# Optimization experiments

Measured on AMD Instinct MI355X. Metric: run time of the kernel, lower is better.

## Reference

```python
import jax, jax.numpy as jnp
import numpy as np

NUM_HEADS = 12
TEMPORAL_RES = 8


def _ln(x, g, b, eps=1e-5):
    mu = jnp.mean(x, axis=-1, keepdims=True)
    var = jnp.mean((x - mu) ** 2, axis=-1, keepdims=True)
    return (x - mu) * jax.lax.rsqrt(var + eps) * g + b


def setup_inputs() -> dict:
    key = jax.random.key(0)
    ks = jax.random.split(key, 8)
    s = 0.02
    d = 768
    inp = {
        'box_tensors': jax.random.uniform(ks[0], (16, 16, 10, 4), dtype=jnp.float32),
        'box_categories': jax.random.normal(ks[1], (16, 10, d), dtype=jnp.float32) * s,
        'w1': jax.random.normal(ks[2], (4, d // 2), dtype=jnp.float32) * s,
        'w2': jax.random.normal(ks[3], (d // 2, d), dtype=jnp.float32) * s,
        'ln1_g': jnp.ones((d,), jnp.float32),
        'ln1_b': jnp.zeros((d,), jnp.float32),
        'wqkv': jax.random.normal(ks[4], (d, 3 * d), dtype=jnp.float32) * s,
        'wo': jax.random.normal(ks[5], (d, d), dtype=jnp.float32) * s,
        'bo': jnp.zeros((d,), jnp.float32),
        'ln2_g': jnp.ones((d,), jnp.float32),
        'ln2_b': jnp.zeros((d,), jnp.float32),
        'wfc1': jax.random.normal(ks[6], (d, 4 * d), dtype=jnp.float32) * s,
        'bfc1': jnp.zeros((4 * d,), jnp.float32),
        'wfc2': jax.random.normal(ks[7], (4 * d, d), dtype=jnp.float32) * s,
        'bfc2': jnp.zeros((d,), jnp.float32),
        'H': 14,
        'W': 14,
    }
    return inp


def _forward(box_tensors, box_categories, w1, w2, ln1_g, ln1_b, wqkv, wo, bo,
             ln2_g, ln2_b, wfc1, bfc1, wfc2, bfc2, H, W):
    B, T, O, _ = box_tensors.shape
    d = box_categories.shape[-1]
    # coord -> feature MLP (no biases), then pos-emb add
    h = jax.nn.relu(box_tensors @ w1)
    x = jax.nn.relu(h @ w2)                      # [B,T,O,d]
    x = x + box_categories[None]                 # broadcast over batch
    L = T * O
    x = x.reshape(B, L, d)
    # --- self-attention block (pre-LN ViT style) ---
    hn = _ln(x, ln1_g, ln1_b)
    qkv = (hn @ wqkv).reshape(B, L, 3, NUM_HEADS, d // NUM_HEADS)
    q, k, v = qkv[:, :, 0], qkv[:, :, 1], qkv[:, :, 2]   # [B,L,h,dh]
    scale = 1.0 / jnp.sqrt(jnp.asarray(d // NUM_HEADS, x.dtype))
    att = jnp.einsum('bqhd,bkhd->bhqk', q, k) * scale
    att = jax.nn.softmax(att, axis=-1)
    o = jnp.einsum('bhqk,bkhd->bqhd', att, v).reshape(B, L, d)
    x = x + (o @ wo + bo)
    hn = _ln(x, ln2_g, ln2_b)
    x = x + (jax.nn.gelu(hn @ wfc1 + bfc1, approximate=False) @ wfc2 + bfc2)
    feats = x.reshape(B, T, O, d)
    # --- box2spatial layout scatter: sum each object's feature into grid cells inside its box ---
    x1 = jnp.minimum(box_tensors[..., 0], box_tensors[..., 2])
    x2 = jnp.maximum(box_tensors[..., 0], box_tensors[..., 2])
    y1 = jnp.minimum(box_tensors[..., 1], box_tensors[..., 3])
    y2 = jnp.maximum(box_tensors[..., 1], box_tensors[..., 3])
    cy = (jnp.arange(H, dtype=x.dtype) + 0.5) / H    # [H]
    cx = (jnp.arange(W, dtype=x.dtype) + 0.5) / W    # [W]
    in_y = (cy[None, None, None, :] >= y1[..., None]) & (cy[None, None, None, :] <= y2[..., None])  # [B,T,O,H]
    in_x = (cx[None, None, None, :] >= x1[..., None]) & (cx[None, None, None, :] <= x2[..., None])  # [B,T,O,W]
    mask = (in_y[..., :, None] & in_x[..., None, :]).astype(x.dtype)  # [B,T,O,H,W]
    grid = jnp.einsum('btohw,btod->bthwd', mask, feats)               # [B,T,H,W,d]
    # temporal avg pooling to TEMPORAL_RES frames
    Tr = T // TEMPORAL_RES
    if Tr > 1:
        grid = grid.reshape(B, T // Tr, Tr, H, W, d).mean(axis=2)
    return grid.reshape(B, -1, d)                 # [B, T'*H*W, d]


def reference(box_tensors, box_categories, w1, w2, ln1_g, ln1_b, wqkv, wo, bo,
              ln2_g, ln2_b, wfc1, bfc1, wfc2, bfc2, H, W):
    return _forward(box_tensors, box_categories, w1, w2, ln1_g, ln1_b, wqkv, wo, bo,
                    ln2_g, ln2_b, wfc1, bfc1, wfc2, bfc2, H, W)
```

## Files before the change

kernel.cpp:

```cpp
#include <hip/hip_runtime.h>
#include <hip/hip_bf16.h>
#include <math.h>


#define BATCH 16
#define TT    16
#define OO    10
#define LL    160
#define BL    2560
#define DD    768
#define NH    12
#define DH    64
#define GH    14
#define GW    14
#define TGRP  8

typedef unsigned short ushort_t;
typedef __attribute__((ext_vector_type(8))) __bf16 bf16x8;
typedef __attribute__((ext_vector_type(4))) float f32x4;

__device__ __forceinline__ ushort_t f2bf(float f) {
    unsigned int u = __float_as_uint(f);
    u += 0x7fffu + ((u >> 16) & 1u);
    return (ushort_t)(u >> 16);
}

__global__ __launch_bounds__(256)
void transpose_w(const float* __restrict__ W, ushort_t* __restrict__ Wt, int K, int N)
{
    __shared__ float s[32][33];
    const int n0 = blockIdx.x * 32, k0 = blockIdx.y * 32;
    const int tx = threadIdx.x & 31, ty = threadIdx.x >> 5;
#pragma unroll
    for (int r = 0; r < 4; ++r)
        s[ty + r * 8][tx] = W[(size_t)(k0 + ty + r * 8) * N + n0 + tx];
    __syncthreads();
#pragma unroll
    for (int r = 0; r < 4; ++r)
        Wt[(size_t)(n0 + ty + r * 8) * K + k0 + tx] = f2bf(s[tx][ty + r * 8]);
}

__global__ __launch_bounds__(256)
void box_h(const float* __restrict__ box, const float* __restrict__ w1,
           ushort_t* __restrict__ h)
{
    const int idx = blockIdx.x * 256 + threadIdx.x;
    const int r = idx / 384, j = idx - r * 384;
    const float* bx = box + (size_t)r * 4;
    float v = bx[0] * w1[j] + bx[1] * w1[384 + j] +
              bx[2] * w1[768 + j] + bx[3] * w1[1152 + j];
    h[idx] = f2bf(fmaxf(v, 0.f));
}

__global__ __launch_bounds__(256)
void ln_kernel(const float* __restrict__ in, const float* __restrict__ g,
               const float* __restrict__ bvec, ushort_t* __restrict__ out)
{
    const int r = blockIdx.x;
    const int tid = threadIdx.x;
    const float* row = in + (size_t)r * DD;
    float v0 = row[tid], v1 = row[tid + 256], v2 = row[tid + 512];
    float s  = v0 + v1 + v2;
    float s2 = v0 * v0 + v1 * v1 + v2 * v2;
#pragma unroll
    for (int off = 32; off > 0; off >>= 1) {
        s  += __shfl_down(s, off);
        s2 += __shfl_down(s2, off);
    }
    __shared__ float red[8];
    int wave = tid >> 6, lane = tid & 63;
    if (lane == 0) { red[wave] = s; red[wave + 4] = s2; }
    __syncthreads();
    s  = red[0] + red[1] + red[2] + red[3];
    s2 = red[4] + red[5] + red[6] + red[7];
    float mu  = s * (1.f / DD);
    float var = s2 * (1.f / DD) - mu * mu;
    float inv = rsqrtf(var + 1e-5f);
    ushort_t* op = out + (size_t)r * DD;
    op[tid]       = f2bf((v0 - mu) * inv * g[tid]       + bvec[tid]);
    op[tid + 256] = f2bf((v1 - mu) * inv * g[tid + 256] + bvec[tid + 256]);
    op[tid + 512] = f2bf((v2 - mu) * inv * g[tid + 512] + bvec[tid + 512]);
}

#define LOADF(aa, bb, kk)                                                        \
    _Pragma("unroll")                                                            \
    for (int i = 0; i < 4; ++i) {                                                \
        aa[i] = *reinterpret_cast<const bf16x8*>(ap + (size_t)(i * 16) * lda + (kk)); \
        bb[i] = *reinterpret_cast<const bf16x8*>(bp + (size_t)(i * 16) * ldb + (kk)); \
    }
#define MFMA16(aa, bb)                                                           \
    _Pragma("unroll")                                                            \
    for (int i = 0; i < 4; ++i)                                                  \
        _Pragma("unroll")                                                        \
        for (int j = 0; j < 4; ++j)                                              \
            acc[i][j] = __builtin_amdgcn_mfma_f32_16x16x32_bf16(aa[i], bb[j], acc[i][j], 0, 0, 0);

template <int MODE, int SPLIT>
__global__ __launch_bounds__(64)
void gemm_rf(const ushort_t* __restrict__ A, int lda,
             const ushort_t* __restrict__ Bt, int ldb,
             const float* __restrict__ bias, const float* __restrict__ cat,
             float* __restrict__ Cf, ushort_t* __restrict__ Cb,
             int ldc, int K)
{
    const int lane = threadIdx.x;
    const int l16 = lane & 15, quad = lane >> 4;
    const int row0 = blockIdx.y * 64, col0 = blockIdx.x * 64;
    const int Kper = K / SPLIT;
    const int k0 = blockIdx.z * Kper;

    const ushort_t* ap = A  + (size_t)(row0 + l16) * lda + k0 + quad * 8;
    const ushort_t* bp = Bt + (size_t)(col0 + l16) * ldb + k0 + quad * 8;

    f32x4 acc[4][4];
#pragma unroll
    for (int i = 0; i < 4; ++i)
#pragma unroll
        for (int j = 0; j < 4; ++j) {
            acc[i][j][0] = 0.f; acc[i][j][1] = 0.f;
            acc[i][j][2] = 0.f; acc[i][j][3] = 0.f;
        }

    bf16x8 a0[4], b0[4], a1[4], b1[4];
    LOADF(a0, b0, 0)
    int kt = 0;
    for (; kt + 64 < Kper; kt += 64) {
        LOADF(a1, b1, kt + 32)
        MFMA16(a0, b0)
        LOADF(a0, b0, kt + 64)
        MFMA16(a1, b1)
    }
    LOADF(a1, b1, kt + 32)
    MFMA16(a0, b0)
    MFMA16(a1, b1)

    const int q4 = quad * 4;
#pragma unroll
    for (int i = 0; i < 4; ++i)
#pragma unroll
        for (int j = 0; j < 4; ++j) {
            const int gcol = col0 + j * 16 + l16;
            const float bj = (MODE == 1 || MODE == 2)
                               ? ((SPLIT == 1 || blockIdx.z == 0) ? bias[gcol] : 0.f)
                               : 0.f;
#pragma unroll
            for (int r = 0; r < 4; ++r) {
                const int grow = row0 + i * 16 + q4 + r;
                const size_t idx = (size_t)grow * ldc + gcol;
                const float v = acc[i][j][r];
                if (MODE == 1) {
                    if (SPLIT > 1) atomicAdd(&Cf[idx], v + bj);
                    else           Cf[idx] += v + bj;
                } else if (MODE == 2) {
                    const float u = v + bj;
                    Cb[idx] = f2bf(0.5f * u * (1.f + erff(u * 0.70710678118654752f)));
                } else if (MODE == 3) {
                    Cb[idx] = f2bf(v);
                } else {
                    Cf[idx] = fmaxf(v, 0.f) + cat[(size_t)(grow % LL) * DD + gcol];
                }
            }
        }
}

#define KS_STRIDE 72
#define VT_STRIDE 168
__global__ __launch_bounds__(320)
void attention_mfma(ushort_t* __restrict__ qkv)
{
    __shared__ ushort_t Ks[160 * KS_STRIDE];
    __shared__ ushort_t Vt[64 * VT_STRIDE];
    __shared__ ushort_t Pb[5][32 * VT_STRIDE];

    const int b  = blockIdx.x / NH;
    const int hh = blockIdx.x % NH;
    ushort_t* basew = qkv + (size_t)b * LL * (3 * DD) + hh * DH;
    const ushort_t* base = basew;
    const int tid  = threadIdx.x;
    const int wave = tid >> 6, lane = tid & 63;
    const int l16 = lane & 15, quad = lane >> 4;

#pragma unroll
    for (int it = 0; it < 4; ++it) {
        int idx = tid + it * 320;
        int l = idx >> 3, c8 = (idx & 7) * 8;
        uint4 kv = *(const uint4*)(base + (size_t)l * (3 * DD) + DD + c8);
        *(uint4*)&Ks[l * KS_STRIDE + c8] = kv;
        uint4 vv = *(const uint4*)(base + (size_t)l * (3 * DD) + 2 * DD + c8);
        ushort_t e[8];
        *(uint4*)e = vv;
#pragma unroll
        for (int i = 0; i < 8; ++i)
            Vt[(c8 + i) * VT_STRIDE + l] = e[i];
    }

    const int q0 = wave * 32;
    bf16x8 qf[2][2];
#pragma unroll
    for (int t = 0; t < 2; ++t)
#pragma unroll
        for (int k = 0; k < 2; ++k)
            qf[t][k] = *reinterpret_cast<const bf16x8*>(
                base + (size_t)(q0 + t * 16 + l16) * (3 * DD) + k * 32 + quad * 8);

    __syncthreads();

    f32x4 S0[10], S1[10];
#pragma unroll
    for (int nt = 0; nt < 10; ++nt) {
        f32x4 z = {0.f, 0.f, 0.f, 0.f};
        const ushort_t* kb = &Ks[(nt * 16 + l16) * KS_STRIDE + quad * 8];
        bf16x8 kf0 = *reinterpret_cast<const bf16x8*>(kb);
        bf16x8 kf1 = *reinterpret_cast<const bf16x8*>(kb + 32);
        f32x4 a0 = __builtin_amdgcn_mfma_f32_16x16x32_bf16(qf[0][0], kf0, z, 0, 0, 0);
        S0[nt]   = __builtin_amdgcn_mfma_f32_16x16x32_bf16(qf[0][1], kf1, a0, 0, 0, 0);
        f32x4 a1 = __builtin_amdgcn_mfma_f32_16x16x32_bf16(qf[1][0], kf0, z, 0, 0, 0);
        S1[nt]   = __builtin_amdgcn_mfma_f32_16x16x32_bf16(qf[1][1], kf1, a1, 0, 0, 0);
    }

#pragma unroll
    for (int t = 0; t < 2; ++t) {
        f32x4* S = t ? S1 : S0;
        float mrow[4] = {-1e30f, -1e30f, -1e30f, -1e30f};
#pragma unroll
        for (int nt = 0; nt < 10; ++nt)
#pragma unroll
            for (int r = 0; r < 4; ++r) {
                S[nt][r] *= 0.125f;
                mrow[r] = fmaxf(mrow[r], S[nt][r]);
            }
#pragma unroll
        for (int r = 0; r < 4; ++r) {
            mrow[r] = fmaxf(mrow[r], __shfl_xor(mrow[r], 1));
            mrow[r] = fmaxf(mrow[r], __shfl_xor(mrow[r], 2));
            mrow[r] = fmaxf(mrow[r], __shfl_xor(mrow[r], 4));
            mrow[r] = fmaxf(mrow[r], __shfl_xor(mrow[r], 8));
        }
        float lsum[4] = {0.f, 0.f, 0.f, 0.f};
#pragma unroll
        for (int nt = 0; nt < 10; ++nt)
#pragma unroll
            for (int r = 0; r < 4; ++r) {
                float e = __expf(S[nt][r] - mrow[r]);
                S[nt][r] = e;
                lsum[r] += e;
            }
#pragma unroll
        for (int r = 0; r < 4; ++r) {
            lsum[r] += __shfl_xor(lsum[r], 1);
            lsum[r] += __shfl_xor(lsum[r], 2);
            lsum[r] += __shfl_xor(lsum[r], 4);
            lsum[r] += __shfl_xor(lsum[r], 8);
            lsum[r] = 1.f / lsum[r];
        }
#pragma unroll
        for (int nt = 0; nt < 10; ++nt)
#pragma unroll
            for (int r = 0; r < 4; ++r)
                Pb[wave][(t * 16 + quad * 4 + r) * VT_STRIDE + nt * 16 + l16] =
                    f2bf(S[nt][r] * lsum[r]);
    }
    asm volatile("s_waitcnt lgkmcnt(0)" ::: "memory");

#pragma unroll
    for (int dt = 0; dt < 4; ++dt) {
        f32x4 o0 = {0.f, 0.f, 0.f, 0.f}, o1 = {0.f, 0.f, 0.f, 0.f};
#pragma unroll
        for (int ks = 0; ks < 5; ++ks) {
            bf16x8 vf = *reinterpret_cast<const bf16x8*>(
                &Vt[(dt * 16 + l16) * VT_STRIDE + ks * 32 + quad * 8]);
            bf16x8 p0 = *reinterpret_cast<const bf16x8*>(
                &Pb[wave][(l16) * VT_STRIDE + ks * 32 + quad * 8]);
            bf16x8 p1 = *reinterpret_cast<const bf16x8*>(
                &Pb[wave][(16 + l16) * VT_STRIDE + ks * 32 + quad * 8]);
            o0 = __builtin_amdgcn_mfma_f32_16x16x32_bf16(vf, p0, o0, 0, 0, 0);
            o1 = __builtin_amdgcn_mfma_f32_16x16x32_bf16(vf, p1, o1, 0, 0, 0);
        }
#pragma unroll
        for (int t = 0; t < 2; ++t) {
            f32x4 o = t ? o1 : o0;
            ushort_t pk[4];
#pragma unroll
            for (int r = 0; r < 4; ++r) pk[r] = f2bf(o[r]);
            ushort_t* dst = basew + (size_t)(q0 + t * 16 + l16) * (3 * DD) +
                            dt * 16 + quad * 4;
            *(uint2*)dst = *(const uint2*)pk;
        }
    }
}

__global__ __launch_bounds__(256)
void mask_grid(const float* __restrict__ box, const float* __restrict__ feats,
               float* __restrict__ out)
{
    const int hw = blockIdx.x;
    const int g  = blockIdx.y;
    const int b  = blockIdx.z;
    const int hh = hw / GW, w = hw % GW;
    const float cy = (hh + 0.5f) / (float)GH;
    const float cx = (w  + 0.5f) / (float)GW;
    const int tid = threadIdx.x;

    __shared__ float flg[20];
    if (tid < 20) {
        int t = g * 2 + tid / OO, o = tid % OO;
        const float* bx = box + (size_t)((b * TT + t) * OO + o) * 4;
        float x1 = fminf(bx[0], bx[2]), x2 = fmaxf(bx[0], bx[2]);
        float y1 = fminf(bx[1], bx[3]), y2 = fmaxf(bx[1], bx[3]);
        flg[tid] = (cy >= y1 && cy <= y2 && cx >= x1 && cx <= x2) ? 1.f : 0.f;
    }
    __syncthreads();

    float a0 = 0.f, a1 = 0.f, a2 = 0.f;
#pragma unroll
    for (int p = 0; p < 20; ++p) {
        if (flg[p] != 0.f) {
            int r = (b * TT + g * 2 + p / OO) * OO + (p % OO);
            const float* f = feats + (size_t)r * DD;
            a0 += f[tid]; a1 += f[tid + 256]; a2 += f[tid + 512];
        }
    }
    float* op = out + ((size_t)b * (TGRP * GH * GW) + g * (GH * GW) + hw) * DD;
    op[tid]       = a0 * 0.5f;
    op[tid + 256] = a1 * 0.5f;
    op[tid + 512] = a2 * 0.5f;
}

extern "C" void kernel_launch(void* const* d_in, const int* in_sizes, int n_in,
                              void* d_out, int out_size, void* d_ws, size_t ws_size,
                              hipStream_t stream)
{
    const float* box  = (const float*)d_in[0];
    const float* cat  = (const float*)d_in[1];
    const float* w1   = (const float*)d_in[2];
    const float* w2   = (const float*)d_in[3];
    const float* ln1g = (const float*)d_in[4];
    const float* ln1b = (const float*)d_in[5];
    const float* wqkv = (const float*)d_in[6];
    const float* wo   = (const float*)d_in[7];
    const float* bo   = (const float*)d_in[8];
    const float* ln2g = (const float*)d_in[9];
    const float* ln2b = (const float*)d_in[10];
    const float* wfc1 = (const float*)d_in[11];
    const float* bfc1 = (const float*)d_in[12];
    const float* wfc2 = (const float*)d_in[13];
    const float* bfc2 = (const float*)d_in[14];
    float* out = (float*)d_out;

    char* wsb = (char*)d_ws;
    float*    x     = (float*)   (wsb + 0);
    ushort_t* qkvb  = (ushort_t*)(wsb + 7864320);
    ushort_t* fc1b  = qkvb;
    ushort_t* hnb   = (ushort_t*)(wsb + 23592960);
    ushort_t* wqkvT = (ushort_t*)(wsb + 27525120);
    ushort_t* woT   = (ushort_t*)(wsb + 31064064);
    ushort_t* wfc1T = (ushort_t*)(wsb + 32243712);
    ushort_t* wfc2T = (ushort_t*)(wsb + 36962304);
    ushort_t* w2T   = (ushort_t*)(wsb + 41680896);
    ushort_t* h     = (ushort_t*)(wsb + 42270720);

    transpose_w<<<dim3(2304 / 32, 768 / 32), 256, 0, stream>>>(wqkv, wqkvT, 768, 2304);
    transpose_w<<<dim3(768 / 32, 768 / 32), 256, 0, stream>>>(wo, woT, 768, 768);
    transpose_w<<<dim3(3072 / 32, 768 / 32), 256, 0, stream>>>(wfc1, wfc1T, 768, 3072);
    transpose_w<<<dim3(768 / 32, 3072 / 32), 256, 0, stream>>>(wfc2, wfc2T, 3072, 768);
    transpose_w<<<dim3(768 / 32, 384 / 32), 256, 0, stream>>>(w2, w2T, 384, 768);

    box_h<<<BL * 384 / 256, 256, 0, stream>>>(box, w1, h);
    gemm_rf<4, 1><<<dim3(12, 40, 1), 64, 0, stream>>>(h, 384, w2T, 384, nullptr, cat,
                                                      x, nullptr, DD, 384);
    ln_kernel<<<BL, 256, 0, stream>>>(x, ln1g, ln1b, hnb);
    gemm_rf<3, 1><<<dim3(36, 40, 1), 64, 0, stream>>>(hnb, DD, wqkvT, DD, nullptr, nullptr,
                                                      nullptr, qkvb, 3 * DD, DD);
    attention_mfma<<<BATCH * NH, 320, 0, stream>>>(qkvb);
    gemm_rf<1, 2><<<dim3(12, 40, 2), 64, 0, stream>>>(qkvb, 3 * DD, woT, DD, bo, nullptr,
                                                      x, nullptr, DD, DD);
    ln_kernel<<<BL, 256, 0, stream>>>(x, ln2g, ln2b, hnb);
    gemm_rf<2, 1><<<dim3(48, 40, 1), 64, 0, stream>>>(hnb, DD, wfc1T, DD, bfc1, nullptr,
                                                      nullptr, fc1b, 4 * DD, DD);
    gemm_rf<1, 4><<<dim3(12, 40, 4), 64, 0, stream>>>(fc1b, 4 * DD, wfc2T, 4 * DD, bfc2, nullptr,
                                                      x, nullptr, DD, 4 * DD);
    mask_grid<<<dim3(GH * GW, TGRP, BATCH), 256, 0, stream>>>(box, x, out);
}
```

Baseline: 372.2 us.

## Replace register-only GEMMs with LDS-staged 128x128 double-buffered MFMA GEMM

Adds a new GEMM kernel in which each 256-thread block computes a 128x128 tile. Its A and B K-slices are staged into shared memory with global_load_lds async copies and double buffered, so the next slice loads while MFMA runs on the current one. The four transformer GEMMs (QKV, out-proj, FC1, FC2) switch to this kernel from the 64-thread register-fed version. The aim is more operand reuse across waves and less global traffic, at the cost of fewer, larger blocks and a per-step barrier.

```diff
diff --git a/kernel.cpp b/kernel.cpp
--- a/kernel.cpp
+++ b/kernel.cpp
@@ -163,6 +163,107 @@
         }
 }
 
+#define GLL(gp, lp) __builtin_amdgcn_global_load_lds(                       \
+    (const __attribute__((address_space(1))) void*)(gp),                     \
+    (__attribute__((address_space(3))) void*)(lp), 16, 0, 0)
+
+template <int MODE, int SPLIT>
+__global__ __launch_bounds__(256)
+void gemm_lds(const ushort_t* __restrict__ A, int lda,
+              const ushort_t* __restrict__ Bt, int ldb,
+              const float* __restrict__ bias,
+              float* __restrict__ Cf, ushort_t* __restrict__ Cb,
+              int ldc, int K)
+{
+    __shared__ ushort_t As[2][4096];
+    __shared__ ushort_t Bs[2][4096];
+
+    const int t    = threadIdx.x;
+    const int wv   = t >> 6;
+    const int lane = t & 63;
+    const int l16  = lane & 15, quad = lane >> 4;
+    const int wr   = (wv >> 1) * 64;
+    const int wc   = (wv & 1) * 64;
+
+    const int row0 = blockIdx.y * 128, col0 = blockIdx.x * 128;
+    const int Kper = K / SPLIT;
+    const int k0   = blockIdx.z * Kper;
+    const int steps = Kper / 32;
+
+    const int srow  = t & 127;
+    const int skq0  = t >> 7;
+    const ushort_t* Ag = A  + (size_t)(row0 + srow) * lda + k0 + skq0 * 8;
+    const ushort_t* Bg = Bt + (size_t)(col0 + srow) * ldb + k0 + skq0 * 8;
+
+#define STAGE(c, kk) do {                                                    \
+        GLL(Ag + (kk),      &As[c][wv * 512]);                               \
+        GLL(Ag + (kk) + 16, &As[c][2048 + wv * 512]);                        \
+        GLL(Bg + (kk),      &Bs[c][wv * 512]);                               \
+        GLL(Bg + (kk) + 16, &Bs[c][2048 + wv * 512]);                        \
+    } while (0)
+
+    f32x4 acc[4][4];
+#pragma unroll
+    for (int i = 0; i < 4; ++i)
+#pragma unroll
+        for (int j = 0; j < 4; ++j) {
+            acc[i][j][0] = 0.f; acc[i][j][1] = 0.f;
+            acc[i][j][2] = 0.f; acc[i][j][3] = 0.f;
+        }
+
+    STAGE(0, 0);
+    __syncthreads();
+    int cur = 0;
+    for (int s = 0; s < steps; ++s) {
+        if (s + 1 < steps) STAGE(cur ^ 1, (s + 1) * 32);
+        bf16x8 af[4], bfr[4];
+#pragma unroll
+        for (int i = 0; i < 4; ++i)
+            af[i] = *reinterpret_cast<const bf16x8*>(
+                &As[cur][quad * 1024 + (wr + i * 16 + l16) * 8]);
+#pragma unroll
+        for (int j = 0; j < 4; ++j)
+            bfr[j] = *reinterpret_cast<const bf16x8*>(
+                &Bs[cur][quad * 1024 + (wc + j * 16 + l16) * 8]);
+#pragma unroll
+        for (int i = 0; i < 4; ++i)
+#pragma unroll
+            for (int j = 0; j < 4; ++j)
+                acc[i][j] = __builtin_amdgcn_mfma_f32_16x16x32_bf16(
+                    af[i], bfr[j], acc[i][j], 0, 0, 0);
+        __syncthreads();
+        cur ^= 1;
+    }
+#undef STAGE
+
+    const int q4 = quad * 4;
+    const int r0w = row0 + wr, c0w = col0 + wc;
+#pragma unroll
+    for (int i = 0; i < 4; ++i)
+#pragma unroll
+        for (int j = 0; j < 4; ++j) {
+            const int gcol = c0w + j * 16 + l16;
+            const float bj = (MODE == 1 || MODE == 2)
+                               ? ((SPLIT == 1 || blockIdx.z == 0) ? bias[gcol] : 0.f)
+                               : 0.f;
+#pragma unroll
+            for (int r = 0; r < 4; ++r) {
+                const int grow = r0w + i * 16 + q4 + r;
+                const size_t idx = (size_t)grow * ldc + gcol;
+                const float v = acc[i][j][r];
+                if (MODE == 1) {
+                    if (SPLIT > 1) atomicAdd(&Cf[idx], v + bj);
+                    else           Cf[idx] += v + bj;
+                } else if (MODE == 2) {
+                    const float u = v + bj;
+                    Cb[idx] = f2bf(0.5f * u * (1.f + erff(u * 0.70710678118654752f)));
+                } else {
+                    Cb[idx] = f2bf(v);
+                }
+            }
+        }
+}
+
 #define KS_STRIDE 72
 #define VT_STRIDE 168
 __global__ __launch_bounds__(320)
@@ -369,15 +470,15 @@
     gemm_rf<4, 1><<<dim3(12, 40, 1), 64, 0, stream>>>(h, 384, w2T, 384, nullptr, cat,
                                                       x, nullptr, DD, 384);
     ln_kernel<<<BL, 256, 0, stream>>>(x, ln1g, ln1b, hnb);
-    gemm_rf<3, 1><<<dim3(36, 40, 1), 64, 0, stream>>>(hnb, DD, wqkvT, DD, nullptr, nullptr,
-                                                      nullptr, qkvb, 3 * DD, DD);
+    gemm_lds<3, 1><<<dim3(2304 / 128, 2560 / 128, 1), 256, 0, stream>>>(
+        hnb, DD, wqkvT, DD, nullptr, nullptr, qkvb, 3 * DD, DD);
     attention_mfma<<<BATCH * NH, 320, 0, stream>>>(qkvb);
-    gemm_rf<1, 2><<<dim3(12, 40, 2), 64, 0, stream>>>(qkvb, 3 * DD, woT, DD, bo, nullptr,
-                                                      x, nullptr, DD, DD);
+    gemm_lds<1, 2><<<dim3(768 / 128, 2560 / 128, 2), 256, 0, stream>>>(
+        qkvb, 3 * DD, woT, DD, bo, x, nullptr, DD, DD);
     ln_kernel<<<BL, 256, 0, stream>>>(x, ln2g, ln2b, hnb);
-    gemm_rf<2, 1><<<dim3(48, 40, 1), 64, 0, stream>>>(hnb, DD, wfc1T, DD, bfc1, nullptr,
-                                                      nullptr, fc1b, 4 * DD, DD);
-    gemm_rf<1, 4><<<dim3(12, 40, 4), 64, 0, stream>>>(fc1b, 4 * DD, wfc2T, 4 * DD, bfc2, nullptr,
-                                                      x, nullptr, DD, 4 * DD);
+    gemm_lds<2, 1><<<dim3(3072 / 128, 2560 / 128, 1), 256, 0, stream>>>(
+        hnb, DD, wfc1T, DD, bfc1, nullptr, fc1b, 4 * DD, DD);
+    gemm_lds<1, 4><<<dim3(768 / 128, 2560 / 128, 4), 256, 0, stream>>>(
+        fc1b, 4 * DD, wfc2T, 4 * DD, bfc2, x, nullptr, DD, 4 * DD);
     mask_grid<<<dim3(GH * GW, TGRP, BATCH), 256, 0, stream>>>(box, x, out);
 }
```

After: 334.0 us. 10.3% less time.
